# Optimization experiments

Hardware: AMD Instinct MI355X
Metric: run time of the kernel (lower is better)

## Reference

```python
import jax, jax.numpy as jnp
import numpy as np

BN_EPS = 1e-5
R = 8.0        # radius
L = 11         # sequence kernel size (odd), s = L//2
K = 24         # kernel_channels[-1]
N_NODES = 32768
N_EDGES = 524288
C_IN = 128     # in_channels == out_channels
C_W = 32       # width = out_channels * base_width / 64


def _bn(x, gamma, beta):
    # BatchNorm1d in training mode: biased batch statistics over node dim
    mu = jnp.mean(x, axis=0)
    var = jnp.mean(jnp.square(x - mu), axis=0)
    return (x - mu) * jax.lax.rsqrt(var + BN_EPS) * gamma + beta


def _lrelu(x, slope):
    return jnp.where(x >= 0, x, slope * x)


def setup_inputs() -> dict:
    key = jax.random.key(0)
    ks = jax.random.split(key, 10)

    def glorot(k, shape, fan_in):
        return jax.random.normal(k, shape, jnp.float32) * np.float32(1.0 / np.sqrt(fan_in))

    inp = {}
    inp["x"] = jax.random.normal(ks[0], (N_NODES, C_IN), jnp.float32)
    inp["pos"] = jax.random.normal(ks[1], (N_NODES, 3), jnp.float32) * 10.0
    inp["ori"] = jax.random.normal(ks[2], (N_NODES, 9), jnp.float32)
    inp["seq"] = jnp.arange(N_NODES, dtype=jnp.int32)
    inp["edge_index"] = jax.random.randint(ks[3], (2, N_EDGES), 0, N_NODES, jnp.int32)
    # input MLP params: BN(C_IN) -> LeakyReLU(0.1) -> Linear(C_IN->C_W, no bias) -> BN(C_W) -> LeakyReLU(0.1)
    inp["bn1_g"] = jnp.ones((C_IN,), jnp.float32)
    inp["bn1_b"] = jnp.zeros((C_IN,), jnp.float32)
    inp["lin1_w"] = glorot(ks[4], (C_IN, C_W), C_IN)
    inp["bn2_g"] = jnp.ones((C_W,), jnp.float32)
    inp["bn2_b"] = jnp.zeros((C_W,), jnp.float32)
    # CDConv WeightNet (single layer kernel_channels=[K]): per-seq-bin affine 7 -> K
    inp["wn_w"] = glorot(ks[5], (L, 7, K), 7)
    inp["wn_b"] = jnp.zeros((L, K), jnp.float32)
    # CDConv output projection: [K*C_W, C_W]
    inp["conv_w"] = glorot(ks[6], (K * C_W, C_W), K * C_W)
    # output Linear: BN(C_W) -> LeakyReLU(0.1) -> Linear(C_W->C_IN, no bias)
    inp["bn3_g"] = jnp.ones((C_W,), jnp.float32)
    inp["bn3_b"] = jnp.zeros((C_W,), jnp.float32)
    inp["lin2_w"] = glorot(ks[7], (C_W, C_IN), C_W)
    return inp


def reference(x, pos, ori, seq, edge_index,
              bn1_g, bn1_b, lin1_w, bn2_g, bn2_b,
              wn_w, wn_b, conv_w, bn3_g, bn3_b, lin2_w):
    n = x.shape[0]
    identity = x  # in_channels == out_channels -> identity branch is passthrough

    # ----- input MLP (mid_channels=None) -----
    h = _lrelu(_bn(x, bn1_g, bn1_b), 0.1)
    h = h @ lin1_w                       # [N, C_W]
    h = _lrelu(_bn(h, bn2_g, bn2_b), 0.1)

    # ----- CDConv: continuous geometric kernel over neighbor edges -----
    src, dst = edge_index[0], edge_index[1]      # message j=src -> i=dst
    d = pos[src] - pos[dst]                      # [E,3]
    dist = jnp.linalg.norm(d, axis=-1, keepdims=True)
    direction = d / (dist + 1e-9)
    Ri = ori[dst].reshape(-1, 3, 3)              # receiver local frame
    Rj = ori[src].reshape(-1, 3, 3)
    pos_local = jnp.einsum('eij,ej->ei', Ri, direction)      # direction in local frame
    ori_feat = jnp.einsum('eij,ej->ei', Ri, Rj[:, 0, :])     # neighbor axis in local frame
    delta = jnp.concatenate([pos_local, ori_feat, dist / R], axis=-1)  # [E,7]

    s = L // 2
    sidx = jnp.clip(seq[src] - seq[dst], -s, s) + s          # [E] in [0, L)

    # WeightNet: per-edge affine selected by sequence bin, LeakyReLU(0.2)
    w = _lrelu(jnp.einsum('ef,efk->ek', delta, wn_w[sidx]) + wn_b[sidx], 0.2)  # [E,K]

    # message = outer(kernel_weight, x_j), scatter-sum to receivers
    msg = (w[:, :, None] * h[src][:, None, :]).reshape(w.shape[0], K * C_W)   # [E, K*C_W]
    agg = jax.ops.segment_sum(msg, dst, num_segments=n)                        # [N, K*C_W]
    h = agg @ conv_w                                                            # [N, C_W]

    # ----- output Linear + residual -----
    h = _lrelu(_bn(h, bn3_g, bn3_b), 0.1)
    out = h @ lin2_w + identity
    return out
```

## Files before the change

### kernel.cpp

```cpp
#include <hip/hip_runtime.h>

#define N_NODES 32768
#define C_IN 128
#define C_W 32
#define KK 24
#define SS 5
#define GG 8

#define LD6(W, PTR) do { const float4* _p = (const float4*)(PTR); \
  W[0]=_p[0]; W[1]=_p[1]; W[2]=_p[2]; W[3]=_p[3]; W[4]=_p[4]; W[5]=_p[5]; } while(0)

#define ACC24(W, V) do { float _v = (V); \
  a[0]+=W[0].x*_v;  a[1]+=W[0].y*_v;  a[2]+=W[0].z*_v;  a[3]+=W[0].w*_v;  \
  a[4]+=W[1].x*_v;  a[5]+=W[1].y*_v;  a[6]+=W[1].z*_v;  a[7]+=W[1].w*_v;  \
  a[8]+=W[2].x*_v;  a[9]+=W[2].y*_v;  a[10]+=W[2].z*_v; a[11]+=W[2].w*_v; \
  a[12]+=W[3].x*_v; a[13]+=W[3].y*_v; a[14]+=W[3].z*_v; a[15]+=W[3].w*_v; \
  a[16]+=W[4].x*_v; a[17]+=W[4].y*_v; a[18]+=W[4].z*_v; a[19]+=W[4].w*_v; \
  a[20]+=W[5].x*_v; a[21]+=W[5].y*_v; a[22]+=W[5].z*_v; a[23]+=W[5].w*_v; } while(0)

__global__ void __launch_bounds__(256) k_pre(
        const float* __restrict__ x, float* __restrict__ s1,
        const int* __restrict__ ei, int E, int* __restrict__ counts) {
    int t = threadIdx.x;
    int c = t % C_IN;
    int r0 = blockIdx.x * 2 + t / C_IN;
    float s = 0.f, sq = 0.f;
    for (int r = r0; r < N_NODES; r += 512) {
        float v = x[(size_t)r * C_IN + c];
        s += v; sq += v * v;
    }
    atomicAdd(&s1[c], s);
    atomicAdd(&s1[C_IN + c], sq);
    for (int e = blockIdx.x * 256 + t; e < E; e += 256 * 256)
        atomicAdd(&counts[ei[E + e]], 1);
}

__global__ void __launch_bounds__(256) k_mlp1(
        const float* __restrict__ x, const float* __restrict__ s1,
        const float* __restrict__ g1, const float* __restrict__ b1,
        const float* __restrict__ w1, float* __restrict__ hpre,
        float* __restrict__ s2sh) {
    __shared__ float sAB[2][C_IN];
    __shared__ float sx[32][C_IN + 4];
    __shared__ float sw[C_IN][C_W];
    const int t = threadIdx.x;
    const int row0 = blockIdx.x * 32;
    if (t < C_IN) {
        float mean = s1[t] * (1.f / N_NODES);
        float var = s1[C_IN + t] * (1.f / N_NODES) - mean * mean;
        float a = g1[t] * rsqrtf(var + 1e-5f);
        sAB[0][t] = a; sAB[1][t] = b1[t] - mean * a;
    }
    for (int idx = t; idx < C_IN * C_W; idx += 256)
        sw[idx / C_W][idx % C_W] = w1[idx];
    __syncthreads();
    for (int idx = t; idx < 32 * 32; idx += 256) {
        int r = idx >> 5, cq = idx & 31;
        float4 v = *(const float4*)&x[(size_t)(row0 + r) * C_IN + cq * 4];
        float* d = &sx[r][cq * 4];
        float a0 = sAB[0][cq*4+0]*v.x + sAB[1][cq*4+0];
        float a1 = sAB[0][cq*4+1]*v.y + sAB[1][cq*4+1];
        float a2 = sAB[0][cq*4+2]*v.z + sAB[1][cq*4+2];
        float a3 = sAB[0][cq*4+3]*v.w + sAB[1][cq*4+3];
        d[0] = a0 >= 0.f ? a0 : 0.1f * a0;
        d[1] = a1 >= 0.f ? a1 : 0.1f * a1;
        d[2] = a2 >= 0.f ? a2 : 0.1f * a2;
        d[3] = a3 >= 0.f ? a3 : 0.1f * a3;
    }
    __syncthreads();
    const int r = t >> 3, c0 = (t & 7) * 4;
    float ac0 = 0.f, ac1 = 0.f, ac2 = 0.f, ac3 = 0.f;
    #pragma unroll 8
    for (int cc = 0; cc < C_IN; ++cc) {
        float xv = sx[r][cc];
        float4 wv = *(const float4*)&sw[cc][c0];
        ac0 += xv * wv.x; ac1 += xv * wv.y; ac2 += xv * wv.z; ac3 += xv * wv.w;
    }
    float4 o; o.x = ac0; o.y = ac1; o.z = ac2; o.w = ac3;
    *(float4*)&hpre[(size_t)(row0 + r) * C_W + c0] = o;
    __syncthreads();
    sx[r][c0] = ac0; sx[r][c0+1] = ac1; sx[r][c0+2] = ac2; sx[r][c0+3] = ac3;
    __syncthreads();
    if (t < C_W) {
        float s = 0.f, sq = 0.f;
        #pragma unroll
        for (int rr = 0; rr < 32; ++rr) {
            float v = sx[rr][t];
            s += v; sq += v * v;
        }
        int sh = (blockIdx.x & 7) * 64;
        atomicAdd(&s2sh[sh + t], s);
        atomicAdd(&s2sh[sh + C_W + t], sq);
    }
}

__global__ void __launch_bounds__(1024) k_scan(
        const int* __restrict__ counts, int* __restrict__ offsets,
        int* __restrict__ cursor) {
    __shared__ int sblk[1024];
    const int t = threadIdx.x;
    const int base = t * 32;
    const int4* cp = (const int4*)(counts + base);
    int loc[32];
    int s = 0;
    #pragma unroll
    for (int q = 0; q < 8; ++q) {
        int4 v = cp[q];
        loc[q*4+0] = s; s += v.x;
        loc[q*4+1] = s; s += v.y;
        loc[q*4+2] = s; s += v.z;
        loc[q*4+3] = s; s += v.w;
    }
    sblk[t] = s;
    __syncthreads();
    for (int d = 1; d < 1024; d <<= 1) {
        int u = (t >= d) ? sblk[t - d] : 0;
        __syncthreads();
        sblk[t] += u;
        __syncthreads();
    }
    const int blockbase = sblk[t] - s;
    #pragma unroll
    for (int q = 0; q < 8; ++q) {
        int4 o;
        o.x = blockbase + loc[q*4+0];
        o.y = blockbase + loc[q*4+1];
        o.z = blockbase + loc[q*4+2];
        o.w = blockbase + loc[q*4+3];
        ((int4*)(offsets + base))[q] = o;
        ((int4*)(cursor + base))[q] = o;
    }
    if (t == 1023) offsets[N_NODES] = sblk[1023];
}

__global__ void __launch_bounds__(256) k_edge(
        const int* __restrict__ ei, int E,
        const float* __restrict__ pos, const float* __restrict__ ori,
        const int* __restrict__ seq,
        const float* __restrict__ wnw, const float* __restrict__ wnb,
        int* __restrict__ cursor, int* __restrict__ srcPerm,
        float* __restrict__ wPerm) {
    __shared__ float sWnw[11][169];
    __shared__ float sWnb[11][24];
    const int t = threadIdx.x;
    for (int idx = t; idx < 11 * 168; idx += 256)
        sWnw[idx / 168][idx % 168] = wnw[idx];
    for (int idx = t; idx < 11 * 24; idx += 256)
        sWnb[idx / 24][idx % 24] = wnb[idx];
    __syncthreads();
    const int e = blockIdx.x * 256 + t;
    if (e >= E) return;
    const int src = ei[e];
    const int dst = ei[E + e];
    int ds = seq[src] - seq[dst];
    ds = ds < -SS ? -SS : (ds > SS ? SS : ds);
    const int sb = ds + SS;
    float dx = pos[src * 3 + 0] - pos[dst * 3 + 0];
    float dy = pos[src * 3 + 1] - pos[dst * 3 + 1];
    float dz = pos[src * 3 + 2] - pos[dst * 3 + 2];
    float dist = sqrtf(dx * dx + dy * dy + dz * dz);
    float inv = 1.f / (dist + 1e-9f);
    float ux = dx * inv, uy = dy * inv, uz = dz * inv;
    float b0 = ori[src * 9 + 0], b1 = ori[src * 9 + 1], b2 = ori[src * 9 + 2];
    float delta[7];
    #pragma unroll
    for (int r = 0; r < 3; ++r) {
        float m0 = ori[dst * 9 + r * 3 + 0];
        float m1 = ori[dst * 9 + r * 3 + 1];
        float m2 = ori[dst * 9 + r * 3 + 2];
        delta[r]     = m0 * ux + m1 * uy + m2 * uz;
        delta[3 + r] = m0 * b0 + m1 * b1 + m2 * b2;
    }
    delta[6] = dist * 0.125f;
    float w[KK];
    #pragma unroll
    for (int k = 0; k < KK; ++k) {
        float acc = sWnb[sb][k];
        #pragma unroll
        for (int f = 0; f < 7; ++f)
            acc += delta[f] * sWnw[sb][f * 24 + k];
        w[k] = acc >= 0.f ? acc : 0.2f * acc;
    }
    const int p = atomicAdd(&cursor[dst], 1);
    srcPerm[p] = src;
    float4* wp = (float4*)(wPerm + (size_t)p * KK);
    #pragma unroll
    for (int q = 0; q < 6; ++q) {
        float4 o; o.x = w[q*4]; o.y = w[q*4+1]; o.z = w[q*4+2]; o.w = w[q*4+3];
        wp[q] = o;
    }
}

__global__ void __launch_bounds__(256) k_node(
    const int* __restrict__ offsets, const int* __restrict__ srcPerm,
    const float* __restrict__ wPerm, const float* __restrict__ hpre,
    const float* __restrict__ s2sh, const float* __restrict__ g2,
    const float* __restrict__ b2, const float* __restrict__ convw,
    float* __restrict__ convout, float* __restrict__ s3sh) {
    __shared__ float sA2[C_W], sB2[C_W];
    __shared__ int sOff[GG + 1];
    __shared__ float sAgg[GG][KK * C_W];
    __shared__ float sRv[GG][C_W], sRq[GG][C_W];
    const int i0 = blockIdx.x * GG;
    const int t = threadIdx.x;
    if (t < C_W) {
        float s = 0.f, sq = 0.f;
        #pragma unroll
        for (int j = 0; j < 8; ++j) {
            s  += s2sh[j * 64 + t];
            sq += s2sh[j * 64 + C_W + t];
        }
        float mean = s * (1.f / N_NODES);
        float var = sq * (1.f / N_NODES) - mean * mean;
        float a = g2[t] * rsqrtf(var + 1e-5f);
        sA2[t] = a; sB2[t] = b2[t] - mean * a;
    }
    if (t <= GG) sOff[t] = offsets[i0 + t];
    __syncthreads();
    const int g = t >> 5, c = t & 31;
    const float bnA = sA2[c], bnB = sB2[c];
    const int beg = sOff[g], end = sOff[g + 1];
    float a[KK];
    #pragma unroll
    for (int k = 0; k < KK; ++k) a[k] = 0.f;

    for (int cb = beg; cb < end; cb += 32) {
        const int m = min(32, end - cb);
        int srcL = (cb + c < end) ? srcPerm[cb + c] : 0;
        int j = 0;
        for (; j + 4 <= m; j += 4) {
            int s0 = __shfl(srcL, j + 0, 32);
            int s1 = __shfl(srcL, j + 1, 32);
            int s2 = __shfl(srcL, j + 2, 32);
            int s3 = __shfl(srcL, j + 3, 32);
            float h0 = hpre[(size_t)s0 * C_W + c];
            float h1 = hpre[(size_t)s1 * C_W + c];
            float h2 = hpre[(size_t)s2 * C_W + c];
            float h3 = hpre[(size_t)s3 * C_W + c];
            float4 wa[6], wb[6], wc[6], wd[6];
            const float* wbase = wPerm + (size_t)(cb + j) * KK;
            LD6(wa, wbase);
            LD6(wb, wbase + KK);
            LD6(wc, wbase + 2 * KK);
            LD6(wd, wbase + 3 * KK);
            float v0 = bnA * h0 + bnB; v0 = v0 >= 0.f ? v0 : 0.1f * v0;
            float v1 = bnA * h1 + bnB; v1 = v1 >= 0.f ? v1 : 0.1f * v1;
            float v2 = bnA * h2 + bnB; v2 = v2 >= 0.f ? v2 : 0.1f * v2;
            float v3 = bnA * h3 + bnB; v3 = v3 >= 0.f ? v3 : 0.1f * v3;
            ACC24(wa, v0);
            ACC24(wb, v1);
            ACC24(wc, v2);
            ACC24(wd, v3);
        }
        for (; j < m; ++j) {
            int s0 = __shfl(srcL, j, 32);
            float h0 = hpre[(size_t)s0 * C_W + c];
            float4 wa[6];
            LD6(wa, wPerm + (size_t)(cb + j) * KK);
            float v0 = bnA * h0 + bnB; v0 = v0 >= 0.f ? v0 : 0.1f * v0;
            ACC24(wa, v0);
        }
    }
    #pragma unroll
    for (int k = 0; k < KK; ++k) sAgg[g][k * C_W + c] = a[k];
    __syncthreads();
    float p0 = 0.f, p1 = 0.f;
    for (int r = 0; r < KK * C_W; r += 8) {
        float4 v0 = *(const float4*)&sAgg[g][r];
        float4 v1 = *(const float4*)&sAgg[g][r + 4];
        p0 += v0.x * convw[(r + 0) * 32 + c] + v0.y * convw[(r + 1) * 32 + c]
            + v0.z * convw[(r + 2) * 32 + c] + v0.w * convw[(r + 3) * 32 + c];
        p1 += v1.x * convw[(r + 4) * 32 + c] + v1.y * convw[(r + 5) * 32 + c]
            + v1.z * convw[(r + 6) * 32 + c] + v1.w * convw[(r + 7) * 32 + c];
    }
    float v = p0 + p1;
    convout[(size_t)(i0 + g) * C_W + c] = v;
    sRv[g][c] = v; sRq[g][c] = v * v;
    __syncthreads();
    if (t < 64) {
        int cc = t & 31;
        bool isq = t >= C_W;
        float s = 0.f;
        #pragma unroll
        for (int gg = 0; gg < GG; ++gg)
            s += isq ? sRq[gg][cc] : sRv[gg][cc];
        atomicAdd(&s3sh[(blockIdx.x & 7) * 64 + t], s);
    }
}

__global__ void __launch_bounds__(256) k_out(
        const float* __restrict__ conv, const float* __restrict__ s3sh,
        const float* __restrict__ g3, const float* __restrict__ b3,
        const float* __restrict__ w2, const float* __restrict__ x,
        float* __restrict__ out) {
    __shared__ float sAB[2][C_W];
    __shared__ float sh[8][C_W];
    __shared__ float sw2[C_W][C_IN];
    const int t = threadIdx.x;
    const int row0 = blockIdx.x * 8;
    if (t < C_W) {
        float s = 0.f, sq = 0.f;
        #pragma unroll
        for (int j = 0; j < 8; ++j) {
            s  += s3sh[j * 64 + t];
            sq += s3sh[j * 64 + C_W + t];
        }
        float mean = s * (1.f / N_NODES);
        float var = sq * (1.f / N_NODES) - mean * mean;
        float a = g3[t] * rsqrtf(var + 1e-5f);
        sAB[0][t] = a; sAB[1][t] = b3[t] - mean * a;
    }
    for (int idx = t; idx < C_W * C_IN; idx += 256)
        sw2[idx >> 7][idx & 127] = w2[idx];
    __syncthreads();
    {
        float v = conv[(size_t)row0 * C_W + t];
        int r = t >> 5, cc = t & 31;
        v = sAB[0][cc] * v + sAB[1][cc];
        sh[r][cc] = v >= 0.f ? v : 0.1f * v;
    }
    __syncthreads();
    const int r = t >> 5, c4 = (t & 31) * 4;
    float4 acc = *(const float4*)&x[(size_t)(row0 + r) * C_IN + c4];
    #pragma unroll 8
    for (int cw = 0; cw < C_W; ++cw) {
        float hv = sh[r][cw];
        float4 wv = *(const float4*)&sw2[cw][c4];
        acc.x += hv * wv.x; acc.y += hv * wv.y;
        acc.z += hv * wv.z; acc.w += hv * wv.w;
    }
    *(float4*)&out[(size_t)(row0 + r) * C_IN + c4] = acc;
}

extern "C" void kernel_launch(void* const* d_in, const int* in_sizes, int n_in,
                              void* d_out, int out_size, void* d_ws, size_t ws_size,
                              hipStream_t stream) {
    const float* x     = (const float*)d_in[0];
    const float* pos   = (const float*)d_in[1];
    const float* ori   = (const float*)d_in[2];
    const int*   seq   = (const int*)d_in[3];
    const int*   ei    = (const int*)d_in[4];
    const float* bn1g  = (const float*)d_in[5];
    const float* bn1b  = (const float*)d_in[6];
    const float* lin1w = (const float*)d_in[7];
    const float* bn2g  = (const float*)d_in[8];
    const float* bn2b  = (const float*)d_in[9];
    const float* wnw   = (const float*)d_in[10];
    const float* wnb   = (const float*)d_in[11];
    const float* convw = (const float*)d_in[12];
    const float* bn3g  = (const float*)d_in[13];
    const float* bn3b  = (const float*)d_in[14];
    const float* lin2w = (const float*)d_in[15];
    float* out = (float*)d_out;
    const int E = in_sizes[4] / 2;

    char* wsb = (char*)d_ws;
    size_t off = 0;
    auto alloc = [&](size_t bytes) {
        void* p = wsb + off;
        off = (off + bytes + 255) & ~(size_t)255;
        return p;
    };
    float* s1      = (float*)alloc(256 * 4);
    float* s2sh    = (float*)alloc(512 * 4);
    float* s3sh    = (float*)alloc(512 * 4);
    int*   counts  = (int*)alloc((size_t)N_NODES * 4);
    size_t zero_bytes = off;
    int*   offsets = (int*)alloc(((size_t)N_NODES + 1) * 4);
    int*   cursor  = (int*)alloc((size_t)N_NODES * 4);
    int*   srcPerm = (int*)alloc((size_t)E * 4);
    float* hpre    = (float*)alloc((size_t)N_NODES * C_W * 4);
    float* convo   = (float*)alloc((size_t)N_NODES * C_W * 4);
    float* wPerm   = (float*)alloc((size_t)E * KK * 4);

    hipMemsetAsync(wsb, 0, zero_bytes, stream);

    k_pre<<<256, 256, 0, stream>>>(x, s1, ei, E, counts);
    k_scan<<<1, 1024, 0, stream>>>(counts, offsets, cursor);
    k_edge<<<(E + 255) / 256, 256, 0, stream>>>(ei, E, pos, ori, seq, wnw, wnb,
                                                cursor, srcPerm, wPerm);
    k_mlp1<<<N_NODES / 32, 256, 0, stream>>>(x, s1, bn1g, bn1b, lin1w, hpre, s2sh);
    k_node<<<N_NODES / GG, 256, 0, stream>>>(offsets, srcPerm, wPerm, hpre,
                                             s2sh, bn2g, bn2b, convw, convo, s3sh);
    k_out<<<N_NODES / 8, 256, 0, stream>>>(convo, s3sh, bn3g, bn3b, lin2w, x, out);
}
```

Measured before the change: 286.0 us.

## Restructure node conv projection across threads and reduce register pressure

In k_node, the edge unroll drops from 4 to 2 and launch bounds now request 4 blocks per multiprocessor, which lowers register use so more waves can be resident. The per-node projection by conv_w is reorganised so each thread computes a float4 of outputs over one quarter of the K*C_W reduction, reads conv_w as float4 vectors, and combines the partial sums through a new shared buffer. The sAgg rows are padded to reduce LDS bank conflicts. k_pre is launched with twice as many blocks and its strides are adjusted to match, giving more parallelism for the stats and degree counting at the cost of more atomics.

Result: slower. 293.1 us (+2.5%).

```diff
diff --git a/kernel.cpp b/kernel.cpp
--- a/kernel.cpp
+++ b/kernel.cpp
@@ -6,6 +6,7 @@
 #define KK 24
 #define SS 5
 #define GG 8
+#define AGS (KK * C_W + 4)
 
 #define LD6(W, PTR) do { const float4* _p = (const float4*)(PTR); \
   W[0]=_p[0]; W[1]=_p[1]; W[2]=_p[2]; W[3]=_p[3]; W[4]=_p[4]; W[5]=_p[5]; } while(0)
@@ -25,13 +26,13 @@
     int c = t % C_IN;
     int r0 = blockIdx.x * 2 + t / C_IN;
     float s = 0.f, sq = 0.f;
-    for (int r = r0; r < N_NODES; r += 512) {
+    for (int r = r0; r < N_NODES; r += 1024) {
         float v = x[(size_t)r * C_IN + c];
         s += v; sq += v * v;
     }
     atomicAdd(&s1[c], s);
     atomicAdd(&s1[C_IN + c], sq);
-    for (int e = blockIdx.x * 256 + t; e < E; e += 256 * 256)
+    for (int e = blockIdx.x * 256 + t; e < E; e += 512 * 256)
         atomicAdd(&counts[ei[E + e]], 1);
 }
 
@@ -191,7 +192,7 @@
     }
 }
 
-__global__ void __launch_bounds__(256) k_node(
+__global__ void __launch_bounds__(256, 4) k_node(
     const int* __restrict__ offsets, const int* __restrict__ srcPerm,
     const float* __restrict__ wPerm, const float* __restrict__ hpre,
     const float* __restrict__ s2sh, const float* __restrict__ g2,
@@ -199,7 +200,8 @@
     float* __restrict__ convout, float* __restrict__ s3sh) {
     __shared__ float sA2[C_W], sB2[C_W];
     __shared__ int sOff[GG + 1];
-    __shared__ float sAgg[GG][KK * C_W];
+    __shared__ float sAgg[GG][AGS];
+    __shared__ float sRed[4][GG][C_W];
     __shared__ float sRv[GG][C_W], sRq[GG][C_W];
     const int i0 = blockIdx.x * GG;
     const int t = threadIdx.x;
@@ -228,31 +230,21 @@
         const int m = min(32, end - cb);
         int srcL = (cb + c < end) ? srcPerm[cb + c] : 0;
         int j = 0;
-        for (; j + 4 <= m; j += 4) {
+        for (; j + 2 <= m; j += 2) {
             int s0 = __shfl(srcL, j + 0, 32);
             int s1 = __shfl(srcL, j + 1, 32);
-            int s2 = __shfl(srcL, j + 2, 32);
-            int s3 = __shfl(srcL, j + 3, 32);
             float h0 = hpre[(size_t)s0 * C_W + c];
             float h1 = hpre[(size_t)s1 * C_W + c];
-            float h2 = hpre[(size_t)s2 * C_W + c];
-            float h3 = hpre[(size_t)s3 * C_W + c];
-            float4 wa[6], wb[6], wc[6], wd[6];
+            float4 wa[6], wb[6];
             const float* wbase = wPerm + (size_t)(cb + j) * KK;
             LD6(wa, wbase);
             LD6(wb, wbase + KK);
-            LD6(wc, wbase + 2 * KK);
-            LD6(wd, wbase + 3 * KK);
             float v0 = bnA * h0 + bnB; v0 = v0 >= 0.f ? v0 : 0.1f * v0;
             float v1 = bnA * h1 + bnB; v1 = v1 >= 0.f ? v1 : 0.1f * v1;
-            float v2 = bnA * h2 + bnB; v2 = v2 >= 0.f ? v2 : 0.1f * v2;
-            float v3 = bnA * h3 + bnB; v3 = v3 >= 0.f ? v3 : 0.1f * v3;
             ACC24(wa, v0);
             ACC24(wb, v1);
-            ACC24(wc, v2);
-            ACC24(wd, v3);
-        }
-        for (; j < m; ++j) {
+        }
+        if (j < m) {
             int s0 = __shfl(srcL, j, 32);
             float h0 = hpre[(size_t)s0 * C_W + c];
             float4 wa[6];
@@ -264,18 +256,34 @@
     #pragma unroll
     for (int k = 0; k < KK; ++k) sAgg[g][k * C_W + c] = a[k];
     __syncthreads();
-    float p0 = 0.f, p1 = 0.f;
-    for (int r = 0; r < KK * C_W; r += 8) {
-        float4 v0 = *(const float4*)&sAgg[g][r];
-        float4 v1 = *(const float4*)&sAgg[g][r + 4];
-        p0 += v0.x * convw[(r + 0) * 32 + c] + v0.y * convw[(r + 1) * 32 + c]
-            + v0.z * convw[(r + 2) * 32 + c] + v0.w * convw[(r + 3) * 32 + c];
-        p1 += v1.x * convw[(r + 4) * 32 + c] + v1.y * convw[(r + 5) * 32 + c]
-            + v1.z * convw[(r + 6) * 32 + c] + v1.w * convw[(r + 7) * 32 + c];
-    }
-    float v = p0 + p1;
-    convout[(size_t)(i0 + g) * C_W + c] = v;
-    sRv[g][c] = v; sRq[g][c] = v * v;
+
+    {
+        const int coq = t & 7;
+        const int gp  = (t >> 3) & 7;
+        const int sl  = t >> 6;
+        const int r0  = sl * 192;
+        float4 acc; acc.x = acc.y = acc.z = acc.w = 0.f;
+        #pragma unroll 4
+        for (int rc = 0; rc < 192; rc += 4) {
+            const float4 s4 = *(const float4*)&sAgg[gp][r0 + rc];
+            const float4 w0 = *(const float4*)&convw[(size_t)(r0+rc+0)*32 + coq*4];
+            const float4 w1 = *(const float4*)&convw[(size_t)(r0+rc+1)*32 + coq*4];
+            const float4 w2 = *(const float4*)&convw[(size_t)(r0+rc+2)*32 + coq*4];
+            const float4 w3 = *(const float4*)&convw[(size_t)(r0+rc+3)*32 + coq*4];
+            acc.x += s4.x*w0.x + s4.y*w1.x + s4.z*w2.x + s4.w*w3.x;
+            acc.y += s4.x*w0.y + s4.y*w1.y + s4.z*w2.y + s4.w*w3.y;
+            acc.z += s4.x*w0.z + s4.y*w1.z + s4.z*w2.z + s4.w*w3.z;
+            acc.w += s4.x*w0.w + s4.y*w1.w + s4.z*w2.w + s4.w*w3.w;
+        }
+        *(float4*)&sRed[sl][gp][coq * 4] = acc;
+    }
+    __syncthreads();
+    {
+        const int gg = t >> 5, co = t & 31;
+        float v = sRed[0][gg][co] + sRed[1][gg][co] + sRed[2][gg][co] + sRed[3][gg][co];
+        convout[(size_t)(i0 + gg) * C_W + co] = v;
+        sRv[gg][co] = v; sRq[gg][co] = v * v;
+    }
     __syncthreads();
     if (t < 64) {
         int cc = t & 31;
@@ -375,7 +383,7 @@
 
     hipMemsetAsync(wsb, 0, zero_bytes, stream);
 
-    k_pre<<<256, 256, 0, stream>>>(x, s1, ei, E, counts);
+    k_pre<<<512, 256, 0, stream>>>(x, s1, ei, E, counts);
     k_scan<<<1, 1024, 0, stream>>>(counts, offsets, cursor);
     k_edge<<<(E + 255) / 256, 256, 0, stream>>>(ei, E, pos, ori, seq, wnw, wnb,
                                                 cursor, srcPerm, wPerm);
```
